# Kernel optimization log

Hardware: AMD Instinct MI355X
Metric: run time of the kernel (lower is better)

## Reference

```python
import jax, jax.numpy as jnp
import numpy as np
from jax import lax

NGTH = 15  # num_gth_mem
EPS = 1e-5  # BatchNorm eps


def _conv(x, w, b):
    y = lax.conv_general_dilated(x, w, (1, 1), 'VALID',
                                 dimension_numbers=('NCHW', 'OIHW', 'NCHW'))
    return y + b[None, :, None, None]


def _bn(x, g, b, m, v):
    # eval-mode BatchNorm2d with running stats
    return g[None, :, None, None] * (x - m[None, :, None, None]) * lax.rsqrt(v[None, :, None, None] + EPS) + b[None, :, None, None]


def _masked_stats(x, w):
    # x: (B, M, ...) ; w: (B, M) float weights. Population mean/std over masked mem slots.
    extra = (1,) * (x.ndim - 2)
    we = w.reshape(w.shape[:2] + extra)
    cnt = jnp.sum(w, axis=1).reshape((w.shape[0],) + extra)
    s = jnp.sum(x * we, axis=1)
    ss = jnp.sum(x * x * we, axis=1)
    mean = s / cnt
    var = jnp.maximum(ss / cnt - mean * mean, 0.0)
    return mean, jnp.sqrt(var)


def _forward(target_scores, ptm, pmt, predicted_iou, mem_mask, params):
    nf, ns, nmem, c, h, w = ptm.shape
    B = nf * ns
    ts = target_scores.reshape(B, 1, h, w)
    pmt = pmt.reshape(B, nmem, 1, h, w)
    ptm = ptm.reshape(B, nmem, c, h, w)
    mask = mem_mask.reshape(B, nmem)
    piou = predicted_iou.reshape(B, 1, 1, 1)

    mf = mask.astype(ts.dtype)
    # rank of each selected slot within the masked (ordered) selection
    rank = jnp.cumsum(mf, axis=1) - 1.0
    gth_w = mf * (rank < NGTH).astype(ts.dtype)   # first NGTH selected slots
    oth_w = mf * (rank >= NGTH).astype(ts.dtype)  # remaining selected slots

    max_ts = jnp.max(ts.reshape(B, -1), axis=1)

    pmt_mean, pmt_std = _masked_stats(pmt, mf)                 # (B,1,h,w)
    pmt_gth = pmt[:, :NGTH]                                    # unmasked slice (as in torch code)
    pmt_gth_mean = jnp.mean(pmt_gth, axis=1)
    pmt_gth_std = jnp.std(pmt_gth, axis=1)
    pmt_oth_mean, pmt_oth_std = _masked_stats(pmt, oth_w)

    ptm_max = jnp.max(ptm.reshape(B, nmem, -1), axis=2)        # (B, nmem)
    m_mm, s_mm = _masked_stats(ptm_max, mf)
    m_gm, s_gm = _masked_stats(ptm_max, gth_w)
    m_om, s_om = _masked_stats(ptm_max, oth_w)

    def bcast(v):
        return jnp.broadcast_to(v.reshape(B, 1, 1, 1), (B, 1, h, w))

    inp = jnp.concatenate([
        bcast(max_ts), jnp.broadcast_to(piou, (B, 1, h, w)),
        pmt_mean, pmt_std, pmt_gth_mean, pmt_gth_std, pmt_oth_mean, pmt_oth_std,
        bcast(m_mm), bcast(s_mm), bcast(m_gm), bcast(s_gm), bcast(m_om), bcast(s_om)
    ], axis=1)  # (B, 14, h, w)

    (c1w, c1b, g1, b1, m1, v1, c2w, c2b, g2, b2, m2, v2,
     c3w, c3b, g3, b3, m3, v3, c4w, c4b) = params
    x = jax.nn.relu(_bn(_conv(inp, c1w, c1b), g1, b1, m1, v1))
    x = lax.reduce_window(x, -jnp.inf, lax.max, (1, 1, 2, 2), (1, 1, 2, 2), 'VALID')
    x = jax.nn.relu(_bn(_conv(x, c2w, c2b), g2, b2, m2, v2))
    x = jax.nn.relu(_bn(_conv(x, c3w, c3b), g3, b3, m3, v3))
    x = _conv(x, c4w, c4b)
    return jnp.max(x, axis=(2, 3), keepdims=True)  # AdaptiveMaxPool2d((1,1)) -> (B,1,1,1)


def setup_inputs() -> dict:
    key = jax.random.key(0)
    ks = jax.random.split(key, 16)
    nf, ns, nmem, h, w = 16, 32, 30, 32, 32
    d = {}
    d['target_scores'] = jax.random.normal(ks[0], (nf, ns, 1, h, w), jnp.float32)
    d['ptm'] = jax.random.uniform(ks[1], (nf, ns, nmem, 1, h, w), jnp.float32)
    d['pmt'] = jax.random.uniform(ks[2], (nf, ns, nmem, 1, h, w), jnp.float32)
    d['predicted_iou'] = jax.random.uniform(ks[3], (nf, ns), jnp.float32)
    mask = jax.random.uniform(ks[4], (nf, ns, nmem)) < 0.7
    mask = mask.at[..., :20].set(True)  # >= 20 selected -> 'other' set non-empty
    d['mem_mask'] = mask
    d['conv1_w'] = jax.random.normal(ks[5], (64, 14, 3, 3), jnp.float32) * 0.1
    d['conv1_b'] = jnp.zeros((64,), jnp.float32)
    d['bn1_g'] = jnp.ones((64,), jnp.float32); d['bn1_b'] = jnp.zeros((64,), jnp.float32)
    d['bn1_m'] = jnp.zeros((64,), jnp.float32); d['bn1_v'] = jnp.ones((64,), jnp.float32)
    d['conv2_w'] = jax.random.normal(ks[6], (64, 64, 3, 3), jnp.float32) * 0.05
    d['conv2_b'] = jnp.zeros((64,), jnp.float32)
    d['bn2_g'] = jnp.ones((64,), jnp.float32); d['bn2_b'] = jnp.zeros((64,), jnp.float32)
    d['bn2_m'] = jnp.zeros((64,), jnp.float32); d['bn2_v'] = jnp.ones((64,), jnp.float32)
    d['conv3_w'] = jax.random.normal(ks[7], (64, 64, 3, 3), jnp.float32) * 0.05
    d['conv3_b'] = jnp.zeros((64,), jnp.float32)
    d['bn3_g'] = jnp.ones((64,), jnp.float32); d['bn3_b'] = jnp.zeros((64,), jnp.float32)
    d['bn3_m'] = jnp.zeros((64,), jnp.float32); d['bn3_v'] = jnp.ones((64,), jnp.float32)
    d['conv4_w'] = jax.random.normal(ks[8], (1, 64, 3, 3), jnp.float32) * 0.05
    d['conv4_b'] = jnp.zeros((1,), jnp.float32)
    return d


def reference(target_scores, ptm, pmt, predicted_iou, mem_mask,
              conv1_w, conv1_b, bn1_g, bn1_b, bn1_m, bn1_v,
              conv2_w, conv2_b, bn2_g, bn2_b, bn2_m, bn2_v,
              conv3_w, conv3_b, bn3_g, bn3_b, bn3_m, bn3_v,
              conv4_w, conv4_b):
    params = (conv1_w, conv1_b, bn1_g, bn1_b, bn1_m, bn1_v,
              conv2_w, conv2_b, bn2_g, bn2_b, bn2_m, bn2_v,
              conv3_w, conv3_b, bn3_g, bn3_b, bn3_m, bn3_v,
              conv4_w, conv4_b)
    return _forward(target_scores, ptm, pmt, predicted_iou, mem_mask, params)
```

## Files before the change

### kernel.cpp

```cpp
#include <hip/hip_runtime.h>
#include <math.h>

#define NFB  512
#define NMEM 30
#define PIX  1024
#define EPSF 1e-5f

typedef _Float16 half8_t __attribute__((ext_vector_type(8)));
typedef _Float16 half4_t __attribute__((ext_vector_type(4)));
typedef float float4_t __attribute__((ext_vector_type(4)));

#define OFF_SCAL  8388608
#define OFF_W2R   13631488
#define OFF_W3R   13705216
#define OFF_WR1   13778944
#define OFF_WSUM1 13791232

#define PROC4(CC, BASE)                                              \
  _Pragma("unroll")                                                  \
  for (int j = 0; j < 6; ++j) {                                      \
    const int mj = (BASE) + j;                                       \
    float wm = ((mwm >> mj) & 1u) ? 1.f : 0.f;                       \
    float wo = ((mwo >> mj) & 1u) ? 1.f : 0.f;                       \
    float xv[4] = {CC[j].x, CC[j].y, CC[j].z, CC[j].w};              \
    _Pragma("unroll")                                                \
    for (int k = 0; k < 4; ++k) {                                    \
      float x = xv[k];                                               \
      sA[k] = fmaf(wm, x, sA[k]); qA[k] = fmaf(wm * x, x, qA[k]);    \
      sO[k] = fmaf(wo, x, sO[k]); qO[k] = fmaf(wo * x, x, qO[k]);    \
      if (mj < 15) { sG[k] += x; qG[k] = fmaf(x, x, qG[k]); }        \
    }                                                                \
  }

__global__ __launch_bounds__(256) void k_stats(
    const float* __restrict__ ts, const float* __restrict__ ptm,
    const float* __restrict__ pmt, const float* __restrict__ piou,
    const int* __restrict__ mask,
    const float* __restrict__ c1w, const float* __restrict__ c2w,
    const float* __restrict__ c3w,
    _Float16* __restrict__ w2rep, _Float16* __restrict__ w3rep,
    _Float16* __restrict__ wr1, float* __restrict__ wsum1,
    _Float16* __restrict__ img, float* __restrict__ scal)
{
  __shared__ float s_pmax[NMEM];
  __shared__ float s_red[4];
  const int bid = blockIdx.x, t = threadIdx.x;

  if (bid < 314) {
    int i = bid * 256 + t;
    if (i < 36864) {
      int kr = i / 12288, rem = i - kr * 12288;
      int oc = rem / 192, k = rem - oc * 192;
      int kc = k >> 6, ci = k & 63;
      w2rep[i] = (_Float16)c2w[((oc * 64 + ci) * 3 + kr) * 3 + kc];
    } else if (i < 73728) {
      int j = i - 36864;
      int kr = j / 12288, rem = j - kr * 12288;
      int oc = rem / 192, k = rem - oc * 192;
      int kc = k >> 6, ci = k & 63;
      w3rep[j] = (_Float16)c3w[((oc * 64 + ci) * 3 + kr) * 3 + kc];
    } else if (i < 79872) {
      int j = i - 73728;
      int kr = j / 2048, rem = j - kr * 2048;
      int oc = rem >> 5, k = rem & 31;
      int kc = k >> 3, ci = k & 7;
      _Float16 v = (_Float16)0.f;
      if (kc < 3 && ci < 6)
        v = (_Float16)c1w[((oc * 14 + (2 + ci)) * 3 + kr) * 3 + kc];
      wr1[j] = v;
    } else if (i < 80384) {
      int j = i - 79872;
      int oc = j >> 3, u = j & 7;
      const int uch[8] = {0, 1, 8, 9, 10, 11, 12, 13};
      const float* wp = c1w + (oc * 14 + uch[u]) * 9;
      float s = 0.f;
      #pragma unroll
      for (int k = 0; k < 9; ++k) s += wp[k];
      wsum1[j] = s;
    }
    return;
  }

  if (bid < 826) {
    const int b = bid - 314;
    const int lane = t & 63, wave = t >> 6;
    {
      const float* pb = ptm + (size_t)b * NMEM * PIX + lane * 4;
      #pragma unroll
      for (int pass = 0; pass < 2; ++pass) {
        float4 u[4][4];
        #pragma unroll
        for (int k = 0; k < 4; ++k) {
          int m = wave + 4 * (pass * 4 + k);
          if (m < NMEM) {
            #pragma unroll
            for (int j = 0; j < 4; ++j)
              u[k][j] = *(const float4*)(pb + (size_t)m * PIX + j * 256);
          }
        }
        #pragma unroll
        for (int k = 0; k < 4; ++k) {
          int m = wave + 4 * (pass * 4 + k);
          if (m < NMEM) {
            float4 v0 = u[k][0], v1_ = u[k][1], v2_ = u[k][2], v3_ = u[k][3];
            float mx = fmaxf(fmaxf(fmaxf(v0.x, v0.y), fmaxf(v0.z, v0.w)),
                             fmaxf(fmaxf(v1_.x, v1_.y), fmaxf(v1_.z, v1_.w)));
            mx = fmaxf(mx, fmaxf(fmaxf(fmaxf(v2_.x, v2_.y), fmaxf(v2_.z, v2_.w)),
                                 fmaxf(fmaxf(v3_.x, v3_.y), fmaxf(v3_.z, v3_.w))));
            #pragma unroll
            for (int off = 32; off > 0; off >>= 1)
              mx = fmaxf(mx, __shfl_down(mx, off, 64));
            if (lane == 0) s_pmax[m] = mx;
          }
        }
      }
    }
    {
      float4 v = ((const float4*)(ts + (size_t)b * PIX))[t];
      float mx = fmaxf(fmaxf(v.x, v.y), fmaxf(v.z, v.w));
      #pragma unroll
      for (int off = 32; off > 0; off >>= 1)
        mx = fmaxf(mx, __shfl_down(mx, off, 64));
      if (lane == 0) s_red[wave] = mx;
    }
    __syncthreads();
    if (t == 0) {
      float maxts = fmaxf(fmaxf(s_red[0], s_red[1]), fmaxf(s_red[2], s_red[3]));
      float cum = 0.f, cm = 0.f, cg = 0.f, co = 0.f;
      float sm = 0, sm2 = 0, sg = 0, sg2 = 0, so = 0, so2 = 0;
      for (int m = 0; m < NMEM; ++m) {
        float f  = (mask[b * NMEM + m] != 0) ? 1.f : 0.f;
        float gg = (cum < 15.f) ? f : 0.f;
        float oo = f - gg;
        cum += f;
        float x = s_pmax[m];
        sm += f * x;  sm2 += f * x * x;
        sg += gg * x; sg2 += gg * x * x;
        so += oo * x; so2 += oo * x * x;
        cm += f; cg += gg; co += oo;
      }
      float a = sm / cm, g = sg / cg, o = so / co;
      float* sc = scal + b * 8;
      sc[0] = maxts; sc[1] = piou[b];
      sc[2] = a; sc[3] = sqrtf(fmaxf(sm2 / cm - a * a, 0.f));
      sc[4] = g; sc[5] = sqrtf(fmaxf(sg2 / cg - g * g, 0.f));
      sc[6] = o; sc[7] = sqrtf(fmaxf(so2 / co - o * o, 0.f));
    }
    return;
  }

  {
    const int b = bid - 826;
    const int p0 = t * 4;
    const float* pb = pmt + (size_t)b * NMEM * PIX + p0;

    float4 c0[6], c1[6], c2[6], c3[6], c4[6];
    #pragma unroll
    for (int j = 0; j < 6; ++j) c0[j] = *(const float4*)(pb + (size_t)j * PIX);
    #pragma unroll
    for (int j = 0; j < 6; ++j) c1[j] = *(const float4*)(pb + (size_t)(6 + j) * PIX);

    unsigned mwm = 0u, mwo = 0u;
    float cum = 0.f, cm = 0.f, co = 0.f;
    for (int m = 0; m < NMEM; ++m) {
      int f = (mask[b * NMEM + m] != 0) ? 1 : 0;
      int oo = (f && (cum >= 15.f)) ? 1 : 0;
      cum += (float)f;
      if (f)  mwm |= (1u << m);
      if (oo) mwo |= (1u << m);
      cm += (float)f; co += (float)oo;
    }

    float sA[4] = {0,0,0,0}, qA[4] = {0,0,0,0};
    float sG[4] = {0,0,0,0}, qG[4] = {0,0,0,0};
    float sO[4] = {0,0,0,0}, qO[4] = {0,0,0,0};

    PROC4(c0, 0)
    #pragma unroll
    for (int j = 0; j < 6; ++j) c2[j] = *(const float4*)(pb + (size_t)(12 + j) * PIX);
    PROC4(c1, 6)
    #pragma unroll
    for (int j = 0; j < 6; ++j) c3[j] = *(const float4*)(pb + (size_t)(18 + j) * PIX);
    PROC4(c2, 12)
    #pragma unroll
    for (int j = 0; j < 6; ++j) c4[j] = *(const float4*)(pb + (size_t)(24 + j) * PIX);
    PROC4(c3, 18)
    PROC4(c4, 24)

    half8_t* ob = (half8_t*)img + (size_t)b * 1024 + p0;
    #pragma unroll
    for (int j = 0; j < 4; ++j) {
      float m0 = sA[j] / cm;    float d0 = sqrtf(fmaxf(qA[j] / cm - m0 * m0, 0.f));
      float m1_ = sG[j] / 15.f; float d1 = sqrtf(fmaxf(qG[j] / 15.f - m1_ * m1_, 0.f));
      float m2_ = sO[j] / co;   float d2 = sqrtf(fmaxf(qO[j] / co - m2_ * m2_, 0.f));
      half8_t v;
      v[0] = (_Float16)m0;  v[1] = (_Float16)d0;
      v[2] = (_Float16)m1_; v[3] = (_Float16)d1;
      v[4] = (_Float16)m2_; v[5] = (_Float16)d2;
      v[6] = (_Float16)0.f; v[7] = (_Float16)0.f;
      ob[j] = v;
    }
  }
}

__global__ __launch_bounds__(256, 2) void k_conv(
    const _Float16* __restrict__ img, const float* __restrict__ scal,
    const _Float16* __restrict__ wr1, const float* __restrict__ wsum1,
    const float* __restrict__ c1b, const float* __restrict__ g1,
    const float* __restrict__ b1, const float* __restrict__ m1,
    const float* __restrict__ v1,
    const _Float16* __restrict__ w2rep,
    const float* __restrict__ c2b, const float* __restrict__ g2,
    const float* __restrict__ b2, const float* __restrict__ m2,
    const float* __restrict__ v2,
    const _Float16* __restrict__ w3rep,
    const float* __restrict__ c3b, const float* __restrict__ g3,
    const float* __restrict__ b3, const float* __restrict__ m3,
    const float* __restrict__ v3,
    const float* __restrict__ c4w, const float* __restrict__ c4b,
    float* __restrict__ out)
{
  __shared__ __align__(16) char s_buf[54144];
  __shared__ float s_red[4], s_scal[8];

  const int b = blockIdx.x, t = threadIdx.x;
  const int lane = t & 63, wave = t >> 6;
  const int n16 = lane & 15, q = lane >> 4;
  _Float16* const IMG = (_Float16*)s_buf;
  _Float16* const X1  = (_Float16*)(s_buf + 16432);
  _Float16* const X2S = (_Float16*)s_buf;
  _Float16* const X3  = (_Float16*)(s_buf + 29520);

  {
    const half8_t* src = (const half8_t*)img + (size_t)b * 1024;
    half8_t* dst = (half8_t*)IMG;
    for (int i = t; i < 1027; i += 256) {
      half8_t v = {(_Float16)0.f,(_Float16)0.f,(_Float16)0.f,(_Float16)0.f,
                   (_Float16)0.f,(_Float16)0.f,(_Float16)0.f,(_Float16)0.f};
      if (i < 1024) v = src[i];
      dst[i] = v;
    }
    if (t < 8) s_scal[t] = scal[b * 8 + t];
  }
  __syncthreads();

  {
    const int ocA = wave * 16 + n16;
    half8_t af[3];
    #pragma unroll
    for (int kr = 0; kr < 3; ++kr)
      af[kr] = *(const half8_t*)(wr1 + (kr * 64 + ocA) * 32 + q * 8);
    const int oc0 = wave * 16 + q * 4;
    float scv[4], shv[4], cst[4];
    #pragma unroll
    for (int rg = 0; rg < 4; ++rg) {
      int oc = oc0 + rg;
      float s = g1[oc] * rsqrtf(v1[oc] + EPSF);
      scv[rg] = s;
      shv[rg] = (c1b[oc] - m1[oc]) * s + b1[oc];
      float c = 0.f;
      #pragma unroll
      for (int u = 0; u < 8; ++u) c = fmaf(wsum1[oc * 8 + u], s_scal[u], c);
      cst[rg] = c;
    }
    #pragma unroll 1
    for (int pr = 0; pr < 15; ++pr) {
      const int r0 = pr * 2;
      float4_t acc[2][2];
      #pragma unroll
      for (int row = 0; row < 2; ++row)
        #pragma unroll
        for (int tt = 0; tt < 2; ++tt)
          acc[row][tt] = (float4_t){0.f, 0.f, 0.f, 0.f};
      #pragma unroll
      for (int row = 0; row < 2; ++row) {
        #pragma unroll
        for (int kr = 0; kr < 3; ++kr) {
          const int ip = (r0 + row + kr) * 32 + n16 + q;
          #pragma unroll
          for (int tt = 0; tt < 2; ++tt) {
            half8_t bf = *(const half8_t*)(IMG + (ip + tt * 16) * 8);
            acc[row][tt] = __builtin_amdgcn_mfma_f32_16x16x32_f16(
                af[kr], bf, acc[row][tt], 0, 0, 0);
          }
        }
      }
      #pragma unroll
      for (int tt = 0; tt < 2; ++tt) {
        float mm[4];
        #pragma unroll
        for (int j = 0; j < 4; ++j) {
          float m = fmaxf(acc[0][tt][j], acc[1][tt][j]);
          mm[j] = fmaxf(m, __shfl_xor(m, 1, 64));
        }
        int pc = tt * 8 + (n16 >> 1);
        if (((n16 & 1) == 0) && pc < 15) {
          half4_t vv;
          #pragma unroll
          for (int rg = 0; rg < 4; ++rg)
            vv[rg] = (_Float16)fmaxf(scv[rg] * (mm[rg] + cst[rg]) + shv[rg], 0.f);
          *(half4_t*)(X1 + (pr * 16 + pc) * 72 + oc0) = vv;
        }
      }
    }
  }
  __syncthreads();

  {
    int base72[11];
    #pragma unroll
    for (int nt = 0; nt < 11; ++nt) {
      int p = nt * 16 + n16;
      int pe = (p < 169) ? p : 168;
      int r = pe / 13, c = pe - r * 13;
      base72[nt] = (r * 16 + c) * 72;
    }
    float4_t acc[11];
    #pragma unroll
    for (int nt = 0; nt < 11; ++nt) acc[nt] = (float4_t){0.f, 0.f, 0.f, 0.f};
    const int ocA = wave * 16 + n16;

    auto mfma_kr = [&](const half8_t (&af)[6], int kr) {
      const int krbase = kr * (16 * 72);
      #pragma unroll
      for (int ks = 0; ks < 6; ++ks) {
        const int k0 = ks * 32 + q * 8;
        const int kadd = krbase + (k0 >> 6) * 72 + (k0 & 63);
        #pragma unroll
        for (int nt = 0; nt < 11; ++nt) {
          half8_t bf = *(const half8_t*)(X1 + base72[nt] + kadd);
          acc[nt] = __builtin_amdgcn_mfma_f32_16x16x32_f16(af[ks], bf, acc[nt], 0, 0, 0);
        }
      }
    };

    half8_t afA[6], afB[6];
    {
      const half8_t* wp = (const half8_t*)(w2rep + (size_t)(0 * 64 + ocA) * 192 + q * 8);
      #pragma unroll
      for (int ks = 0; ks < 6; ++ks) afA[ks] = wp[ks * 4];
    }
    {
      const half8_t* wp = (const half8_t*)(w2rep + (size_t)(1 * 64 + ocA) * 192 + q * 8);
      #pragma unroll
      for (int ks = 0; ks < 6; ++ks) afB[ks] = wp[ks * 4];
      mfma_kr(afA, 0);
    }
    {
      const half8_t* wp = (const half8_t*)(w2rep + (size_t)(2 * 64 + ocA) * 192 + q * 8);
      #pragma unroll
      for (int ks = 0; ks < 6; ++ks) afA[ks] = wp[ks * 4];
      mfma_kr(afB, 1);
    }
    mfma_kr(afA, 2);

    const int ocb = wave * 16 + q * 4;
    float scv[4], shv[4];
    #pragma unroll
    for (int rg = 0; rg < 4; ++rg) {
      int o = ocb + rg;
      float s = g2[o] * rsqrtf(v2[o] + EPSF);
      scv[rg] = s;
      shv[rg] = (c2b[o] - m2[o]) * s + b2[o];
    }
    half4_t vout[11];
    #pragma unroll
    for (int nt = 0; nt < 11; ++nt) {
      #pragma unroll
      for (int rg = 0; rg < 4; ++rg)
        vout[nt][rg] = (_Float16)fmaxf(acc[nt][rg] * scv[rg] + shv[rg], 0.f);
    }
    __syncthreads();
    #pragma unroll
    for (int nt = 0; nt < 11; ++nt) {
      int p = nt * 16 + n16;
      if (p < 169) {
        int r = p / 13, c = p - r * 13;
        *(half4_t*)(X2S + (r * 16 + c) * 72 + ocb) = vout[nt];
      }
    }
  }
  __syncthreads();

  float w4r0 = c4w[t];
  float w4r1 = c4w[256 + t];
  float w4r2 = (t < 64) ? c4w[512 + t] : 0.f;

  {
    int base72[8];
    #pragma unroll
    for (int nt = 0; nt < 8; ++nt) {
      int p = nt * 16 + n16;
      int pe = (p < 121) ? p : 120;
      int r = pe / 11, c = pe - r * 11;
      base72[nt] = (r * 16 + c) * 72;
    }
    float4_t acc[8];
    #pragma unroll
    for (int nt = 0; nt < 8; ++nt) acc[nt] = (float4_t){0.f, 0.f, 0.f, 0.f};
    const int ocA = wave * 16 + n16;

    auto mfma_kr3 = [&](const half8_t (&af)[6], int kr) {
      const int krbase = kr * (16 * 72);
      #pragma unroll
      for (int ks = 0; ks < 6; ++ks) {
        const int k0 = ks * 32 + q * 8;
        const int kadd = krbase + (k0 >> 6) * 72 + (k0 & 63);
        #pragma unroll
        for (int nt = 0; nt < 8; ++nt) {
          half8_t bf = *(const half8_t*)(X2S + base72[nt] + kadd);
          acc[nt] = __builtin_amdgcn_mfma_f32_16x16x32_f16(af[ks], bf, acc[nt], 0, 0, 0);
        }
      }
    };

    half8_t afA[6], afB[6];
    {
      const half8_t* wp = (const half8_t*)(w3rep + (size_t)(0 * 64 + ocA) * 192 + q * 8);
      #pragma unroll
      for (int ks = 0; ks < 6; ++ks) afA[ks] = wp[ks * 4];
    }
    {
      const half8_t* wp = (const half8_t*)(w3rep + (size_t)(1 * 64 + ocA) * 192 + q * 8);
      #pragma unroll
      for (int ks = 0; ks < 6; ++ks) afB[ks] = wp[ks * 4];
      mfma_kr3(afA, 0);
    }
    {
      const half8_t* wp = (const half8_t*)(w3rep + (size_t)(2 * 64 + ocA) * 192 + q * 8);
      #pragma unroll
      for (int ks = 0; ks < 6; ++ks) afA[ks] = wp[ks * 4];
      mfma_kr3(afB, 1);
    }
    mfma_kr3(afA, 2);

    const int ocb = wave * 16 + q * 4;
    float scv[4], shv[4];
    #pragma unroll
    for (int rg = 0; rg < 4; ++rg) {
      int o = ocb + rg;
      float s = g3[o] * rsqrtf(v3[o] + EPSF);
      scv[rg] = s;
      shv[rg] = (c3b[o] - m3[o]) * s + b3[o];
    }
    #pragma unroll
    for (int nt = 0; nt < 8; ++nt) {
      int p = nt * 16 + n16;
      if (p < 121) {
        int r = p / 11, c = p - r * 11;
        half4_t vv;
        #pragma unroll
        for (int rg = 0; rg < 4; ++rg)
          vv[rg] = (_Float16)fmaxf(acc[nt][rg] * scv[rg] + shv[rg], 0.f);
        *(half4_t*)(X3 + (r * 16 + c) * 72 + ocb) = vv;
      }
    }
  }
  __syncthreads();

  {
    float* w4s = (float*)s_buf;
    int i0 = t;        { int ci = i0 / 9, k = i0 - ci * 9; w4s[k * 64 + ci] = w4r0; }
    int i1 = 256 + t;  { int ci = i1 / 9, k = i1 - ci * 9; w4s[k * 64 + ci] = w4r1; }
    if (t < 64) { int i2 = 512 + t; int ci = i2 / 9, k = i2 - ci * 9; w4s[k * 64 + ci] = w4r2; }
  }
  __syncthreads();

  {
    const float* w4s = (const float*)s_buf;
    float val = -INFINITY;
    if (t < 81) {
      const int r = t / 9, c = t - (t / 9) * 9;
      float acc = 0.f;
      #pragma unroll
      for (int kr = 0; kr < 3; ++kr)
        #pragma unroll
        for (int kc = 0; kc < 3; ++kc) {
          const _Float16* ip = X3 + ((r + kr) * 16 + (c + kc)) * 72;
          const float* wk = w4s + (kr * 3 + kc) * 64;
          #pragma unroll
          for (int cig = 0; cig < 8; ++cig) {
            half8_t x = *(const half8_t*)(ip + cig * 8);
            #pragma unroll
            for (int j = 0; j < 8; ++j)
              acc = fmaf((float)x[j], wk[cig * 8 + j], acc);
          }
        }
      val = acc;
    }
    #pragma unroll
    for (int off = 32; off > 0; off >>= 1)
      val = fmaxf(val, __shfl_down(val, off, 64));
    if (lane == 0) s_red[wave] = val;
    __syncthreads();
    if (t == 0)
      out[b] = fmaxf(fmaxf(s_red[0], s_red[1]), fmaxf(s_red[2], s_red[3])) + c4b[0];
  }
}

extern "C" void kernel_launch(void* const* d_in, const int* in_sizes, int n_in,
                              void* d_out, int out_size, void* d_ws, size_t ws_size,
                              hipStream_t stream) {
  const float* ts   = (const float*)d_in[0];
  const float* ptm  = (const float*)d_in[1];
  const float* pmt  = (const float*)d_in[2];
  const float* piou = (const float*)d_in[3];
  const int*   mask = (const int*)d_in[4];
  const float* c1w = (const float*)d_in[5];
  const float* c1b = (const float*)d_in[6];
  const float* g1  = (const float*)d_in[7];
  const float* b1  = (const float*)d_in[8];
  const float* m1  = (const float*)d_in[9];
  const float* v1  = (const float*)d_in[10];
  const float* c2w = (const float*)d_in[11];
  const float* c2b = (const float*)d_in[12];
  const float* g2  = (const float*)d_in[13];
  const float* b2  = (const float*)d_in[14];
  const float* m2  = (const float*)d_in[15];
  const float* v2  = (const float*)d_in[16];
  const float* c3w = (const float*)d_in[17];
  const float* c3b = (const float*)d_in[18];
  const float* g3  = (const float*)d_in[19];
  const float* b3  = (const float*)d_in[20];
  const float* m3  = (const float*)d_in[21];
  const float* v3  = (const float*)d_in[22];
  const float* c4w = (const float*)d_in[23];
  const float* c4b = (const float*)d_in[24];

  char* ws = (char*)d_ws;
  _Float16*  img   = (_Float16*)ws;
  float*     scal  = (float*)(ws + OFF_SCAL);
  _Float16*  w2rep = (_Float16*)(ws + OFF_W2R);
  _Float16*  w3rep = (_Float16*)(ws + OFF_W3R);
  _Float16*  wr1   = (_Float16*)(ws + OFF_WR1);
  float*     wsum1 = (float*)(ws + OFF_WSUM1);

  k_stats<<<1338, 256, 0, stream>>>(
      ts, ptm, pmt, piou, mask, c1w, c2w, c3w,
      w2rep, w3rep, wr1, wsum1, img, scal);
  k_conv<<<NFB, 256, 0, stream>>>(
      img, scal, wr1, wsum1, c1b, g1, b1, m1, v1,
      w2rep, c2b, g2, b2, m2, v2,
      w3rep, c3b, g3, b3, m3, v3,
      c4w, c4b, (float*)d_out);
}
```

Measured before the change: 222.5 us.

## Split ptm max reduction across four blocks per batch and move stats to conv

The per-batch ptm max reduction is now spread over four blocks per batch element instead of one. Each wave handles two memory slots, and the fourth block's spare waves compute the target-score max. The masked mean/std over slot maxima is moved from k_stats into the prologue of k_conv, which reads per-slot maxima from a workspace buffer. This raises the block count and memory-level parallelism for the bandwidth-bound ptm read, at the cost of an extra serial single-thread loop and one more barrier at the start of each conv block.

```diff
diff --git a/kernel.cpp b/kernel.cpp
--- a/kernel.cpp
+++ b/kernel.cpp
@@ -10,7 +10,8 @@
 typedef _Float16 half4_t __attribute__((ext_vector_type(4)));
 typedef float float4_t __attribute__((ext_vector_type(4)));
 
-#define OFF_SCAL  8388608
+#define OFF_PMAX  8404992
+#define OFF_TSMAX 8470528
 #define OFF_W2R   13631488
 #define OFF_W3R   13705216
 #define OFF_WR1   13778944
@@ -32,18 +33,24 @@
     }                                                                \
   }
 
+__device__ __forceinline__ float max16(const float4* u) {
+  float mx = fmaxf(fmaxf(u[0].x, u[0].y), fmaxf(u[0].z, u[0].w));
+  mx = fmaxf(mx, fmaxf(fmaxf(u[1].x, u[1].y), fmaxf(u[1].z, u[1].w)));
+  mx = fmaxf(mx, fmaxf(fmaxf(u[2].x, u[2].y), fmaxf(u[2].z, u[2].w)));
+  mx = fmaxf(mx, fmaxf(fmaxf(u[3].x, u[3].y), fmaxf(u[3].z, u[3].w)));
+  return mx;
+}
+
 __global__ __launch_bounds__(256) void k_stats(
     const float* __restrict__ ts, const float* __restrict__ ptm,
-    const float* __restrict__ pmt, const float* __restrict__ piou,
-    const int* __restrict__ mask,
+    const float* __restrict__ pmt, const int* __restrict__ mask,
     const float* __restrict__ c1w, const float* __restrict__ c2w,
     const float* __restrict__ c3w,
     _Float16* __restrict__ w2rep, _Float16* __restrict__ w3rep,
     _Float16* __restrict__ wr1, float* __restrict__ wsum1,
-    _Float16* __restrict__ img, float* __restrict__ scal)
+    _Float16* __restrict__ img, float* __restrict__ pmax,
+    float* __restrict__ tsmax)
 {
-  __shared__ float s_pmax[NMEM];
-  __shared__ float s_red[4];
   const int bid = blockIdx.x, t = threadIdx.x;
 
   if (bid < 314) {
@@ -81,76 +88,46 @@
     return;
   }
 
-  if (bid < 826) {
-    const int b = bid - 314;
+  if (bid < 2362) {
+    const int j = bid - 314;
+    const int b = j >> 2, part = j & 3;
     const int lane = t & 63, wave = t >> 6;
-    {
-      const float* pb = ptm + (size_t)b * NMEM * PIX + lane * 4;
-      #pragma unroll
-      for (int pass = 0; pass < 2; ++pass) {
-        float4 u[4][4];
-        #pragma unroll
-        for (int k = 0; k < 4; ++k) {
-          int m = wave + 4 * (pass * 4 + k);
-          if (m < NMEM) {
-            #pragma unroll
-            for (int j = 0; j < 4; ++j)
-              u[k][j] = *(const float4*)(pb + (size_t)m * PIX + j * 256);
-          }
-        }
-        #pragma unroll
-        for (int k = 0; k < 4; ++k) {
-          int m = wave + 4 * (pass * 4 + k);
-          if (m < NMEM) {
-            float4 v0 = u[k][0], v1_ = u[k][1], v2_ = u[k][2], v3_ = u[k][3];
-            float mx = fmaxf(fmaxf(fmaxf(v0.x, v0.y), fmaxf(v0.z, v0.w)),
-                             fmaxf(fmaxf(v1_.x, v1_.y), fmaxf(v1_.z, v1_.w)));
-            mx = fmaxf(mx, fmaxf(fmaxf(fmaxf(v2_.x, v2_.y), fmaxf(v2_.z, v2_.w)),
-                                 fmaxf(fmaxf(v3_.x, v3_.y), fmaxf(v3_.z, v3_.w))));
-            #pragma unroll
-            for (int off = 32; off > 0; off >>= 1)
-              mx = fmaxf(mx, __shfl_down(mx, off, 64));
-            if (lane == 0) s_pmax[m] = mx;
-          }
-        }
-      }
-    }
-    {
-      float4 v = ((const float4*)(ts + (size_t)b * PIX))[t];
-      float mx = fmaxf(fmaxf(v.x, v.y), fmaxf(v.z, v.w));
+    const int m0 = part * 8 + wave * 2;
+    if (m0 < NMEM) {
+      const float* p0 = ptm + ((size_t)b * NMEM + m0) * PIX + lane * 4;
+      const float* p1 = p0 + PIX;
+      float4 u0[4], u1[4];
+      #pragma unroll
+      for (int jj = 0; jj < 4; ++jj) u0[jj] = *(const float4*)(p0 + jj * 256);
+      #pragma unroll
+      for (int jj = 0; jj < 4; ++jj) u1[jj] = *(const float4*)(p1 + jj * 256);
+      float mx0 = max16(u0);
+      float mx1 = max16(u1);
+      #pragma unroll
+      for (int off = 32; off > 0; off >>= 1) {
+        mx0 = fmaxf(mx0, __shfl_down(mx0, off, 64));
+        mx1 = fmaxf(mx1, __shfl_down(mx1, off, 64));
+      }
+      if (lane == 0) {
+        pmax[b * 32 + m0]     = mx0;
+        pmax[b * 32 + m0 + 1] = mx1;
+      }
+    } else {
+      const float* p0 = ts + (size_t)b * PIX + lane * 4;
+      float4 u0[4];
+      #pragma unroll
+      for (int jj = 0; jj < 4; ++jj) u0[jj] = *(const float4*)(p0 + jj * 256);
+      float mx = max16(u0);
       #pragma unroll
       for (int off = 32; off > 0; off >>= 1)
         mx = fmaxf(mx, __shfl_down(mx, off, 64));
-      if (lane == 0) s_red[wave] = mx;
-    }
-    __syncthreads();
-    if (t == 0) {
-      float maxts = fmaxf(fmaxf(s_red[0], s_red[1]), fmaxf(s_red[2], s_red[3]));
-      float cum = 0.f, cm = 0.f, cg = 0.f, co = 0.f;
-      float sm = 0, sm2 = 0, sg = 0, sg2 = 0, so = 0, so2 = 0;
-      for (int m = 0; m < NMEM; ++m) {
-        float f  = (mask[b * NMEM + m] != 0) ? 1.f : 0.f;
-        float gg = (cum < 15.f) ? f : 0.f;
-        float oo = f - gg;
-        cum += f;
-        float x = s_pmax[m];
-        sm += f * x;  sm2 += f * x * x;
-        sg += gg * x; sg2 += gg * x * x;
-        so += oo * x; so2 += oo * x * x;
-        cm += f; cg += gg; co += oo;
-      }
-      float a = sm / cm, g = sg / cg, o = so / co;
-      float* sc = scal + b * 8;
-      sc[0] = maxts; sc[1] = piou[b];
-      sc[2] = a; sc[3] = sqrtf(fmaxf(sm2 / cm - a * a, 0.f));
-      sc[4] = g; sc[5] = sqrtf(fmaxf(sg2 / cg - g * g, 0.f));
-      sc[6] = o; sc[7] = sqrtf(fmaxf(so2 / co - o * o, 0.f));
+      if (lane == 0) tsmax[b] = mx;
     }
     return;
   }
 
   {
-    const int b = bid - 826;
+    const int b = bid - 2362;
     const int p0 = t * 4;
     const float* pb = pmt + (size_t)b * NMEM * PIX + p0;
 
@@ -204,7 +181,9 @@
 }
 
 __global__ __launch_bounds__(256, 2) void k_conv(
-    const _Float16* __restrict__ img, const float* __restrict__ scal,
+    const _Float16* __restrict__ img, const float* __restrict__ piou,
+    const int* __restrict__ mask, const float* __restrict__ pmax,
+    const float* __restrict__ tsmax,
     const _Float16* __restrict__ wr1, const float* __restrict__ wsum1,
     const float* __restrict__ c1b, const float* __restrict__ g1,
     const float* __restrict__ b1, const float* __restrict__ m1,
@@ -222,6 +201,7 @@
 {
   __shared__ __align__(16) char s_buf[54144];
   __shared__ float s_red[4], s_scal[8];
+  __shared__ float s_pm[32], s_mf[32], s_ex[2];
 
   const int b = blockIdx.x, t = threadIdx.x;
   const int lane = t & 63, wave = t >> 6;
@@ -240,7 +220,35 @@
       if (i < 1024) v = src[i];
       dst[i] = v;
     }
-    if (t < 8) s_scal[t] = scal[b * 8 + t];
+    if (t < 30) {
+      s_pm[t] = pmax[b * 32 + t];
+      s_mf[t] = (mask[b * NMEM + t] != 0) ? 1.f : 0.f;
+    } else if (t == 30) {
+      s_ex[0] = tsmax[b];
+    } else if (t == 31) {
+      s_ex[1] = piou[b];
+    }
+  }
+  __syncthreads();
+  if (t == 0) {
+    float cum = 0.f, cm = 0.f, cg = 0.f, co = 0.f;
+    float sm = 0, sm2 = 0, sg = 0, sg2 = 0, so = 0, so2 = 0;
+    for (int m = 0; m < NMEM; ++m) {
+      float f  = s_mf[m];
+      float gg = (cum < 15.f) ? f : 0.f;
+      float oo = f - gg;
+      cum += f;
+      float x = s_pm[m];
+      sm += f * x;  sm2 += f * x * x;
+      sg += gg * x; sg2 += gg * x * x;
+      so += oo * x; so2 += oo * x * x;
+      cm += f; cg += gg; co += oo;
+    }
+    float a = sm / cm, g = sg / cg, o = so / co;
+    s_scal[0] = s_ex[0]; s_scal[1] = s_ex[1];
+    s_scal[2] = a; s_scal[3] = sqrtf(fmaxf(sm2 / cm - a * a, 0.f));
+    s_scal[4] = g; s_scal[5] = sqrtf(fmaxf(sg2 / cg - g * g, 0.f));
+    s_scal[6] = o; s_scal[7] = sqrtf(fmaxf(so2 / co - o * o, 0.f));
   }
   __syncthreads();
 
@@ -529,17 +537,19 @@
 
   char* ws = (char*)d_ws;
   _Float16*  img   = (_Float16*)ws;
-  float*     scal  = (float*)(ws + OFF_SCAL);
+  float*     pmax  = (float*)(ws + OFF_PMAX);
+  float*     tsmax = (float*)(ws + OFF_TSMAX);
   _Float16*  w2rep = (_Float16*)(ws + OFF_W2R);
   _Float16*  w3rep = (_Float16*)(ws + OFF_W3R);
   _Float16*  wr1   = (_Float16*)(ws + OFF_WR1);
   float*     wsum1 = (float*)(ws + OFF_WSUM1);
 
-  k_stats<<<1338, 256, 0, stream>>>(
-      ts, ptm, pmt, piou, mask, c1w, c2w, c3w,
-      w2rep, w3rep, wr1, wsum1, img, scal);
+  k_stats<<<2874, 256, 0, stream>>>(
+      ts, ptm, pmt, mask, c1w, c2w, c3w,
+      w2rep, w3rep, wr1, wsum1, img, pmax, tsmax);
   k_conv<<<NFB, 256, 0, stream>>>(
-      img, scal, wr1, wsum1, c1b, g1, b1, m1, v1,
+      img, piou, mask, pmax, tsmax,
+      wr1, wsum1, c1b, g1, b1, m1, v1,
       w2rep, c2b, g2, b2, m2, v2,
       w3rep, c3b, g3, b3, m3, v3,
       c4w, c4b, (float*)d_out);
```

New measurement: 225.8 us. About the same (+1.5%).
